# Kernel tuning notes

Hardware: AMD Instinct MI355X
Metric: run time of the kernel (lower is better)

The kernel has to match this reference:

```python
import jax, jax.numpy as jnp
import numpy as np

N_SUPPORT, N_QUERY, N_CLASS = 10, 25, 2
DIM0, FEAT = 128, 512


def setup_inputs() -> dict:
    key = jax.random.key(0)
    n_items = N_CLASS * N_SUPPORT + N_CLASS * N_QUERY  # 70
    x = jax.random.normal(key, (n_items, DIM0, FEAT), dtype=jnp.float32)
    return {"x": x, "n_support": N_SUPPORT, "n_query": N_QUERY, "n_class": N_CLASS}


def reference(x, n_support, n_query, n_class):
    # Original loops: for each query i (n_class*n_query of them),
    # for each support j in x0 then x1 (2*n_support total, i.e. the first
    # n_class*n_support rows when n_class==2), emit cat([support_j, query_i], -1).
    ns_all = n_class * n_support          # total supports iterated per query
    nq_all = n_class * n_query            # number of queries
    sup = x[:ns_all]                      # [NS, D, F]
    qry = x[ns_all:]                      # [NQ, D, F]
    D, F = x.shape[1], x.shape[2]
    # Broadcast to pairwise grid [NQ, NS, D, F] without python loops.
    sup_b = jnp.broadcast_to(sup[None, :, :, :], (nq_all, ns_all, D, F))
    qry_b = jnp.broadcast_to(qry[:, None, :, :], (nq_all, ns_all, D, F))
    out = jnp.concatenate([sup_b, qry_b], axis=-1)  # [NQ, NS, D, 2F]
    return out.reshape(nq_all * ns_all, D, 2 * F)
```

## Files before the change

kernel.cpp:

```cpp
#include <hip/hip_runtime.h>

#define NS_ALL 20
#define NQ_ALL 50
#define DIM0   128
#define FEAT   512


typedef float f32x4 __attribute__((ext_vector_type(4)));

__global__ __launch_bounds__(256) void concat_pairs_kernel(
    const f32x4* __restrict__ x4, f32x4* __restrict__ out4)
{
    const f32x4* sup4 = x4;
    const f32x4* qry4 = x4 + NS_ALL * DIM0 * (FEAT / 4);

    const int total = NQ_ALL * NS_ALL * DIM0 * (2 * FEAT / 4);
    const int stride = gridDim.x * blockDim.x;

    for (int i = blockIdx.x * blockDim.x + threadIdx.x; i < total; i += stride) {
        int row = i >> 8;
        int c4  = i & 255;
        int q   = row / (NS_ALL * DIM0);
        int rem = row - q * (NS_ALL * DIM0);
        int s   = rem >> 7;
        int d   = rem & 127;

        f32x4 v;
        if (c4 < (FEAT / 4)) {
            v = sup4[(s * DIM0 + d) * (FEAT / 4) + c4];
        } else {
            v = qry4[(q * DIM0 + d) * (FEAT / 4) + (c4 - (FEAT / 4))];
        }
        __builtin_nontemporal_store(v, &out4[i]);
    }
}

extern "C" void kernel_launch(void* const* d_in, const int* in_sizes, int n_in,
                              void* d_out, int out_size, void* d_ws, size_t ws_size,
                              hipStream_t stream) {
    const f32x4* x4 = (const f32x4*)d_in[0];
    f32x4* out4 = (f32x4*)d_out;

    const int threads = 256;
    const int blocks = 2048;
    concat_pairs_kernel<<<blocks, threads, 0, stream>>>(x4, out4);
}
```

Measured before the change: 107.9 us.

## Stage support and query tiles in LDS and reuse across pair outputs

Each block now handles one d-row for a 5-query by 10-support tile. It loads those 15 feature rows into shared memory once, then writes all 50 concatenated output rows from LDS. The old grid-stride loop re-read the source for every output element and did per-element index division, relying on L2 for reuse. This version cuts global reads and index arithmetic. In exchange it adds a __syncthreads, fixes the grid at 2560 blocks, and each block's stores land in rows that are far apart, which may scatter the write pattern.

Result: faster. 88.81 us (-17.7%).

```diff
diff --git a/kernel.cpp b/kernel.cpp
--- a/kernel.cpp
+++ b/kernel.cpp
@@ -8,30 +8,50 @@
 
 typedef float f32x4 __attribute__((ext_vector_type(4)));
 
-__global__ __launch_bounds__(256) void concat_pairs_kernel(
+#define QT 5
+#define ST 10
+#define F4 (FEAT / 4)
+#define LDS_F4 ((QT + ST) * F4)
+
+__global__ __launch_bounds__(256) void concat_pairs_lds_kernel(
     const f32x4* __restrict__ x4, f32x4* __restrict__ out4)
 {
     const f32x4* sup4 = x4;
-    const f32x4* qry4 = x4 + NS_ALL * DIM0 * (FEAT / 4);
+    const f32x4* qry4 = x4 + NS_ALL * DIM0 * F4;
 
-    const int total = NQ_ALL * NS_ALL * DIM0 * (2 * FEAT / 4);
-    const int stride = gridDim.x * blockDim.x;
+    __shared__ f32x4 lds[LDS_F4];
 
-    for (int i = blockIdx.x * blockDim.x + threadIdx.x; i < total; i += stride) {
-        int row = i >> 8;
-        int c4  = i & 255;
-        int q   = row / (NS_ALL * DIM0);
-        int rem = row - q * (NS_ALL * DIM0);
-        int s   = rem >> 7;
-        int d   = rem & 127;
+    const int tid = threadIdx.x;
+    const int bid = blockIdx.x;
+    const int d   = bid & 127;
+    const int tb  = bid >> 7;
+    const int st  = tb & 1;
+    const int qt  = tb >> 1;
 
+    for (int j = tid; j < LDS_F4; j += 256) {
         f32x4 v;
-        if (c4 < (FEAT / 4)) {
-            v = sup4[(s * DIM0 + d) * (FEAT / 4) + c4];
+        if (j < ST * F4) {
+            int s   = j >> 7;
+            int off = j & 127;
+            v = sup4[((st * ST + s) * DIM0 + d) * F4 + off];
         } else {
-            v = qry4[(q * DIM0 + d) * (FEAT / 4) + (c4 - (FEAT / 4))];
+            int jj  = j - ST * F4;
+            int q   = jj >> 7;
+            int off = jj & 127;
+            v = qry4[((qt * QT + q) * DIM0 + d) * F4 + off];
         }
-        __builtin_nontemporal_store(v, &out4[i]);
+        lds[j] = v;
+    }
+    __syncthreads();
+
+    const f32x4* src = (tid < F4) ? &lds[tid] : &lds[ST * F4 + (tid - F4)];
+    #pragma unroll
+    for (int r = 0; r < QT * ST; ++r) {
+        int q = r / ST;
+        int s = r - q * ST;
+        f32x4 v = (tid < F4) ? src[s * F4] : src[q * F4];
+        int pair = (qt * QT + q) * NS_ALL + (st * ST + s);
+        __builtin_nontemporal_store(v, &out4[((pair << 7) + d) * 256 + tid]);
     }
 }
 
@@ -42,6 +62,6 @@
     f32x4* out4 = (f32x4*)d_out;
 
     const int threads = 256;
-    const int blocks = 2048;
-    concat_pairs_kernel<<<blocks, threads, 0, stream>>>(x4, out4);
+    const int blocks = (NQ_ALL / QT) * (NS_ALL / ST) * DIM0;
+    concat_pairs_lds_kernel<<<blocks, threads, 0, stream>>>(x4, out4);
 }
```

## Scatter each input row once to all its output positions instead of gathering

Applied to the files above, without the earlier changes.

Replaces the grid-stride gather loop with one block per input row (support or query). Each block loads its 512-float row once and writes it to every output pair that uses it: 50 positions for a support row, 20 for a query row. This removes the per-element index division and the redundant reads of the input. The cost is that stores become strided across large distances, the work per block is uneven (50 versus 20 stores), and 8960 small 128-thread blocks are launched.

New measurement: 111.2 us. 1.03x slower.

```diff
diff --git a/kernel.cpp b/kernel.cpp
--- a/kernel.cpp
+++ b/kernel.cpp
@@ -3,35 +3,43 @@
 #define NS_ALL 20
 #define NQ_ALL 50
 #define DIM0   128
-#define FEAT   512
+#define F4     128
 
 
 typedef float f32x4 __attribute__((ext_vector_type(4)));
 
-__global__ __launch_bounds__(256) void concat_pairs_kernel(
+#define SUP_BLOCKS (NS_ALL * DIM0)
+#define QRY_BLOCKS (NQ_ALL * DIM0)
+
+__global__ __launch_bounds__(128) void concat_scatter_kernel(
     const f32x4* __restrict__ x4, f32x4* __restrict__ out4)
 {
+    const int tid = threadIdx.x;
+    const int bid = blockIdx.x;
     const f32x4* sup4 = x4;
-    const f32x4* qry4 = x4 + NS_ALL * DIM0 * (FEAT / 4);
+    const f32x4* qry4 = x4 + NS_ALL * DIM0 * F4;
 
-    const int total = NQ_ALL * NS_ALL * DIM0 * (2 * FEAT / 4);
-    const int stride = gridDim.x * blockDim.x;
-
-    for (int i = blockIdx.x * blockDim.x + threadIdx.x; i < total; i += stride) {
-        int row = i >> 8;
-        int c4  = i & 255;
-        int q   = row / (NS_ALL * DIM0);
-        int rem = row - q * (NS_ALL * DIM0);
-        int s   = rem >> 7;
-        int d   = rem & 127;
-
-        f32x4 v;
-        if (c4 < (FEAT / 4)) {
-            v = sup4[(s * DIM0 + d) * (FEAT / 4) + c4];
-        } else {
-            v = qry4[(q * DIM0 + d) * (FEAT / 4) + (c4 - (FEAT / 4))];
+    if (bid < SUP_BLOCKS) {
+        const int s = bid >> 7;
+        const int d = bid & 127;
+        const f32x4 v = sup4[((s << 7) + d) * F4 + tid];
+        int idx = (((s << 7) + d) << 8) + tid;
+        #pragma unroll
+        for (int q = 0; q < NQ_ALL; ++q) {
+            __builtin_nontemporal_store(v, &out4[idx]);
+            idx += NS_ALL * DIM0 * 256;
         }
-        __builtin_nontemporal_store(v, &out4[i]);
+    } else {
+        const int b = bid - SUP_BLOCKS;
+        const int q = b >> 7;
+        const int d = b & 127;
+        const f32x4 v = qry4[((q << 7) + d) * F4 + tid];
+        int idx = ((q * (NS_ALL * DIM0) + d) << 8) + F4 + tid;
+        #pragma unroll
+        for (int s = 0; s < NS_ALL; ++s) {
+            __builtin_nontemporal_store(v, &out4[idx]);
+            idx += DIM0 * 256;
+        }
     }
 }
 
@@ -41,7 +49,7 @@
     const f32x4* x4 = (const f32x4*)d_in[0];
     f32x4* out4 = (f32x4*)d_out;
 
-    const int threads = 256;
-    const int blocks = 2048;
-    concat_pairs_kernel<<<blocks, threads, 0, stream>>>(x4, out4);
+    const int threads = 128;
+    const int blocks = SUP_BLOCKS + QRY_BLOCKS;
+    concat_scatter_kernel<<<blocks, threads, 0, stream>>>(x4, out4);
 }
```
